# Optimization experiments

Measured on AMD Instinct MI355X. Metric: run time of the kernel, lower is better.

The kernel has to match this reference:

```python
import jax, jax.numpy as jnp
import numpy as np
import math

IMAGE_C = 1
IMAGE_W = 28
PIXELS_PER_ROW = IMAGE_W * IMAGE_C
NUM_HEADS = 8
TOP_K = 96
WINDOW_SIZE = 128
NEG_INF = -jnp.inf


def _causal_2d_mask(T):
    idx = jnp.arange(T)
    q_i = (idx // PIXELS_PER_ROW)[:, None]
    q_j = (idx % PIXELS_PER_ROW // IMAGE_C)[:, None]
    q_c = (idx % IMAGE_C)[:, None]
    k_i = (idx // PIXELS_PER_ROW)[None, :]
    k_j = (idx % PIXELS_PER_ROW // IMAGE_C)[None, :]
    k_c = (idx % IMAGE_C)[None, :]
    allowed = (k_i < q_i) | ((k_i == q_i) & (k_j < q_j)) | ((k_i == q_i) & (k_j == q_j) & (k_c <= q_c))
    return jnp.where(allowed, 0.0, NEG_INF)[None, None]  # [1,1,T,T]


def _window_mask(T, window_size):
    idx = jnp.arange(T)
    blocked = idx[None, :] < idx[:, None] - window_size + 1
    return jnp.where(blocked, NEG_INF, 0.0)[None, None]  # [1,1,T,T]


def setup_inputs() -> dict:
    key = jax.random.key(0)
    ks = jax.random.split(key, 10)
    B, T, E = 4, 2048, 512
    H = NUM_HEADS
    s = 0.02
    return {
        "x": jax.random.normal(ks[0], (B, T, E), jnp.float32),
        "Wq": jax.random.normal(ks[1], (E, E), jnp.float32) * s,
        "bq": jnp.zeros((E,), jnp.float32),
        "Wk": jax.random.normal(ks[2], (E, E), jnp.float32) * s,
        "bk": jnp.zeros((E,), jnp.float32),
        "Wv": jax.random.normal(ks[3], (E, E), jnp.float32) * s,
        "bv": jnp.zeros((E,), jnp.float32),
        "Wo": jax.random.normal(ks[4], (E, E), jnp.float32) * s,
        "bo": jnp.zeros((E,), jnp.float32),
        "log_sigma": jnp.full((H, 1, 1), math.log(2.5), jnp.float32),
    }


def reference(x, Wq, bq, Wk, bk, Wv, bv, Wo, bo, log_sigma):
    B, T, E = x.shape
    H = NUM_HEADS
    D = E // H

    def split_heads(y):  # [B,T,E] -> [B,H,T,D]
        return y.reshape(B, T, H, D).transpose(0, 2, 1, 3)

    q = split_heads(x @ Wq.T + bq)
    k = split_heads(x @ Wk.T + bk)
    v = split_heads(x @ Wv.T + bv)

    # Gaussian-kernel (squared-distance) scores: ||q-k||^2 / (-2 sigma^2)
    q_sq = jnp.sum(q * q, axis=-1, keepdims=True)            # [B,H,T,1]
    k_sq = jnp.sum(k * k, axis=-1, keepdims=True).transpose(0, 1, 3, 2)  # [B,H,1,T]
    product = jnp.einsum("bhqd,bhkd->bhqk", q, k)
    dist_sq = q_sq + k_sq - 2.0 * product
    sigma_sq = jnp.exp(2.0 * log_sigma)                       # [H,1,1]
    scores = dist_sq / (-2.0 * sigma_sq)

    scores = scores + _causal_2d_mask(T)
    if WINDOW_SIZE < T:
        scores = scores + _window_mask(T, WINDOW_SIZE)

    if TOP_K < T:
        K_val = min(TOP_K, T)
        # keep only the top-K scores per row (threshold at the K-th value);
        # equivalent to torch's gather/scatter for distinct finite scores
        top_vals = jax.lax.top_k(scores, K_val)[0]            # [B,H,T,K]
        kth = top_vals[..., -1:]
        scores = jnp.where(scores >= kth, scores, NEG_INF)

    probs = jax.nn.softmax(scores, axis=-1)                   # dropout = identity (eval)
    out = jnp.einsum("bhqk,bhkd->bhqd", probs, v)
    out = out.transpose(0, 2, 1, 3).reshape(B, T, E)
    return out @ Wo.T + bo
```

## Files before the change

kernel.cpp:

```cpp
#include <hip/hip_runtime.h>
#include <math.h>

#define T_SEQ   2048
#define EDIM    512
#define NHEADS  8
#define DHEAD   64
#define BATCH   4
#define WIN     128
#define TOPK    96

typedef _Float16 f16;
typedef f16 f16x2 __attribute__((ext_vector_type(2)));
typedef f16 f16x4 __attribute__((ext_vector_type(4)));
typedef f16 f16x8 __attribute__((ext_vector_type(8)));
typedef float f32x4 __attribute__((ext_vector_type(4)));

#define GLD_LDS(gp, lp) \
    __builtin_amdgcn_global_load_lds((const __attribute__((address_space(1))) void*)(gp), \
                                     (__attribute__((address_space(3))) void*)(lp), 16, 0, 0)

__global__ __launch_bounds__(256) void convert_all(
    const float* __restrict__ x,  const float* __restrict__ wq,
    const float* __restrict__ wk, const float* __restrict__ wv,
    const float* __restrict__ wo,
    f16* __restrict__ xh, f16* __restrict__ wqkvh, f16* __restrict__ woh)
{
    long i = ((long)blockIdx.x * 256 + threadIdx.x) * 4;
    const float* src; f16* dst; long off;
    if      (i < 4194304L) { src = x;  dst = xh;             off = i;            }
    else if (i < 4456448L) { src = wq; dst = wqkvh;          off = i - 4194304L; }
    else if (i < 4718592L) { src = wk; dst = wqkvh + 262144; off = i - 4456448L; }
    else if (i < 4980736L) { src = wv; dst = wqkvh + 524288; off = i - 4718592L; }
    else                   { src = wo; dst = woh;            off = i - 4980736L; }
    float4 v = *(const float4*)(src + off);
    f16x4 h; h.x = (f16)v.x; h.y = (f16)v.y; h.z = (f16)v.z; h.w = (f16)v.w;
    *(f16x4*)(dst + off) = h;
}

__global__ __launch_bounds__(256) void ksq_kernel(const f16* __restrict__ kh,
                                                  float* __restrict__ ksqg)
{
    const int i   = blockIdx.x * 256 + threadIdx.x;
    const int row = i >> 2, part = i & 3;
    const f16* p = kh + (size_t)row * 64 + part * 16;
    const f16x8 a = ((const f16x8*)p)[0];
    const f16x8 b = ((const f16x8*)p)[1];
    float s = 0.f;
#pragma unroll
    for (int j = 0; j < 8; j++) {
        const float fa = (float)a[j], fb = (float)b[j];
        s += fa * fa + fb * fb;
    }
    s += __shfl_xor(s, 1);
    s += __shfl_xor(s, 2);
    if (part == 0) ksqg[row] = s;
}

template <int MODE>
__global__ __launch_bounds__(256) void gemm_mfma(
    const f16* __restrict__ A, const f16* __restrict__ W,
    const float* __restrict__ b0, const float* __restrict__ b1,
    const float* __restrict__ b2, float* __restrict__ C0,
    f16* __restrict__ cq, f16* __restrict__ ck, f16* __restrict__ cv)
{
    __shared__ f16 Ash[16 * 512];
    __shared__ f16 Bsh[16 * 512];

    const int tid  = threadIdx.x;
    const int w    = tid >> 6;
    const int lane = tid & 63;
    const int m0   = blockIdx.x * 128;
    const int n0   = blockIdx.y * 128;
    const int K    = 512;
    const int lr   = lane & 15;
    const int lk8  = (lane >> 4) * 8;

    f32x4 acc[4][4];
#pragma unroll
    for (int i = 0; i < 4; i++)
#pragma unroll
        for (int j = 0; j < 4; j++) acc[i][j] = (f32x4){0.f, 0.f, 0.f, 0.f};

    const int wmi = (w & 1) * 4;
    const int wni = (w >> 1) * 4;

    for (int k0 = 0; k0 < K; k0 += 64) {
#pragma unroll
        for (int cc = 0; cc < 4; cc++) {
            const int c  = w * 4 + cc;
            const int ms = c & 7, kp = c >> 3;
            const int kcol = k0 + kp * 32 + lk8;
            GLD_LDS(A + (size_t)(m0 + ms * 16 + lr) * K + kcol, Ash + c * 512);
            GLD_LDS(W + (size_t)(n0 + ms * 16 + lr) * K + kcol, Bsh + c * 512);
        }
        __syncthreads();

#pragma unroll
        for (int kp = 0; kp < 2; kp++) {
            f16x8 af[4], bf[4];
#pragma unroll
            for (int i = 0; i < 4; i++)
                af[i] = *(const f16x8*)(Ash + (kp * 8 + wmi + i) * 512 + lane * 8);
#pragma unroll
            for (int j = 0; j < 4; j++)
                bf[j] = *(const f16x8*)(Bsh + (kp * 8 + wni + j) * 512 + lane * 8);
#pragma unroll
            for (int i = 0; i < 4; i++)
#pragma unroll
                for (int j = 0; j < 4; j++)
                    acc[i][j] = __builtin_amdgcn_mfma_f32_16x16x32_f16(af[i], bf[j], acc[i][j], 0, 0, 0);
        }
        __syncthreads();
    }

    const int quad = lane >> 4;
    if (MODE == 0) {
#pragma unroll
        for (int i = 0; i < 4; i++) {
#pragma unroll
            for (int j = 0; j < 4; j++) {
                const int n  = n0 + (w >> 1) * 64 + j * 16 + lr;
                const float bv = b0[n];
#pragma unroll
                for (int r = 0; r < 4; r++) {
                    const int m = m0 + (w & 1) * 64 + i * 16 + quad * 4 + r;
                    C0[(size_t)m * 512 + n] = acc[i][j][r] + bv;
                }
            }
        }
    } else {
        const int mat = n0 >> 9;
        const float* bias = (mat == 0) ? b0 : ((mat == 1) ? b1 : b2);
#pragma unroll
        for (int i = 0; i < 4; i++) {
#pragma unroll
            for (int j = 0; j < 4; j++) {
                const int n    = n0 + (w >> 1) * 64 + j * 16 + lr;
                const int ncol = n & 511;
                const int h    = ncol >> 6, d = ncol & 63;
                const float bv = bias[ncol];
                if (mat < 2) {
                    f16* dst = (mat == 0) ? cq : ck;
#pragma unroll
                    for (int r = 0; r < 4; r++) {
                        const int m = m0 + (w & 1) * 64 + i * 16 + quad * 4 + r;
                        const int b = m >> 11, t = m & (T_SEQ - 1);
                        dst[((size_t)((b * NHEADS + h) * T_SEQ) + t) * 64 + d] =
                            (f16)(acc[i][j][r] + bv);
                    }
                } else {
                    const int mb = m0 + (w & 1) * 64 + i * 16 + quad * 4;
                    const int b = mb >> 11, t = mb & (T_SEQ - 1);
                    f16x4 pk;
#pragma unroll
                    for (int r = 0; r < 4; r++) pk[r] = (f16)(acc[i][j][r] + bv);
                    *(f16x4*)(cv + ((size_t)((b * NHEADS + h) * 64 + d)) * T_SEQ + t) = pk;
                }
            }
        }
    }
}

__global__ __launch_bounds__(256) void attn_v3(
    const f16* __restrict__ qh, const f16* __restrict__ kh,
    const f16* __restrict__ vtg, const float* __restrict__ ksqg,
    const float* __restrict__ logsig, f16* __restrict__ abh)
{
    __shared__ __align__(16) char smem[75520];
    f16*   Qs   = (f16*)smem;
    f16*   Ks   = (f16*)(smem + 10240);
    f16*   P    = (f16*)smem;
    float* Sc   = (float*)(smem + 40960);
    f16*   Vt   = (f16*)(smem + 40960);
    float* ksqs = (float*)(smem + 74752);

    const int tid = threadIdx.x, w = tid >> 6, lane = tid & 63;
    const int lr = lane & 15, quad = lane >> 4;
    const int q0 = blockIdx.x * 64, bh = blockIdx.y;
    const int h = bh & 7, b = bh >> 3;
    const size_t tb = (size_t)bh * T_SEQ;
    const int ks0 = q0 - 128;

#pragma unroll
    for (int s = 0; s < 2; s++) {
        const int i = tid + 256 * s;
        const int row = i >> 3, ch = i & 7;
        f16x8 v = *(const f16x8*)(qh + (tb + q0 + row) * 64 + ch * 8);
        *(f16x8*)(Qs + row * 80 + ch * 8) = v;
    }
#pragma unroll
    for (int s = 0; s < 6; s++) {
        const int i = tid + 256 * s;
        const int row = i >> 3, ch = i & 7;
        const int kg = ks0 + row;
        f16x8 v = {};
        if (kg >= 0) v = *(const f16x8*)(kh + (tb + kg) * 64 + ch * 8);
        *(f16x8*)(Ks + row * 80 + ch * 8) = v;
    }
    if (tid < 192) {
        const int kg = ks0 + tid;
        ksqs[tid] = (kg >= 0) ? ksqg[tb + kg] : 0.f;
    }
    __syncthreads();

    f32x4 accQ[4][3];
#pragma unroll
    for (int i = 0; i < 4; i++)
#pragma unroll
        for (int jt = 0; jt < 3; jt++) accQ[i][jt] = (f32x4){0.f, 0.f, 0.f, 0.f};

    const int nb = w * 48;
#pragma unroll
    for (int kp = 0; kp < 2; kp++) {
        f16x8 bf[3];
#pragma unroll
        for (int jt = 0; jt < 3; jt++)
            bf[jt] = *(const f16x8*)(Ks + (nb + jt * 16 + lr) * 80 + kp * 32 + quad * 8);
#pragma unroll
        for (int i = 0; i < 4; i++) {
            const f16x8 af = *(const f16x8*)(Qs + (i * 16 + lr) * 80 + kp * 32 + quad * 8);
#pragma unroll
            for (int jt = 0; jt < 3; jt++)
                accQ[i][jt] = __builtin_amdgcn_mfma_f32_16x16x32_f16(af, bf[jt], accQ[i][jt], 0, 0, 0);
        }
    }
    const float inv_s2 = __expf(-2.0f * logsig[h]);
#pragma unroll
    for (int i = 0; i < 4; i++) {
#pragma unroll
        for (int jt = 0; jt < 3; jt++) {
            const int c  = nb + jt * 16 + lr;
            const float kq = ksqs[c];
            const int kg = ks0 + c;
#pragma unroll
            for (int r = 0; r < 4; r++) {
                const int dq = i * 16 + quad * 4 + r;
                const unsigned wc = (unsigned)(c - dq - 1);
                if (wc < 128u) {
                    const float sv = (kg >= 0) ? (accQ[i][jt][r] - 0.5f * kq) * inv_s2
                                               : -INFINITY;
                    Sc[dq * 132 + wc] = sv;
                }
            }
        }
    }
    __syncthreads();

    const int wq = w * 16;
#pragma unroll 1
    for (int qp = 0; qp < 8; qp++) {
        const int dqA = wq + qp * 2, dqB = dqA + 1;
        const float s0A = Sc[dqA * 132 + lane], s1A = Sc[dqA * 132 + 64 + lane];
        const float s0B = Sc[dqB * 132 + lane], s1B = Sc[dqB * 132 + 64 + lane];
        const unsigned b0A = __float_as_uint(s0A), b1A = __float_as_uint(s1A);
        const unsigned b0B = __float_as_uint(s0B), b1B = __float_as_uint(s1B);
        const unsigned u0A = b0A ^ (unsigned)(((int)b0A >> 31) | 0x80000000);
        const unsigned u1A = b1A ^ (unsigned)(((int)b1A >> 31) | 0x80000000);
        const unsigned u0B = b0B ^ (unsigned)(((int)b0B >> 31) | 0x80000000);
        const unsigned u1B = b1B ^ (unsigned)(((int)b1B >> 31) | 0x80000000);
        const float mA = __uint_as_float(__builtin_amdgcn_readlane(__float_as_uint(s1A), 63));
        const float mB = __uint_as_float(__builtin_amdgcn_readlane(__float_as_uint(s1B), 63));

        unsigned tA = 0u, tB = 0u;
#pragma unroll
        for (int bit = 31; bit >= 0; bit--) {
            const unsigned cA = tA | (1u << bit);
            const unsigned cB = tB | (1u << bit);
            const int nA = __popcll(__ballot(u0A >= cA)) + __popcll(__ballot(u1A >= cA));
            const int nB = __popcll(__ballot(u0B >= cB)) + __popcll(__ballot(u1B >= cB));
            if (nA >= TOPK) tA = cA;
            if (nB >= TOPK) tB = cB;
        }

        const float p0A = (u0A >= tA) ? __expf(s0A - mA) : 0.f;
        const float p1A = (u1A >= tA) ? __expf(s1A - mA) : 0.f;
        const float p0B = (u0B >= tB) ? __expf(s0B - mB) : 0.f;
        const float p1B = (u1B >= tB) ? __expf(s1B - mB) : 0.f;

        P[dqA * 200 + dqA + 1 + lane]  = (f16)p0A;
        P[dqA * 200 + dqA + 65 + lane] = (f16)p1A;
        P[dqA * 200 + ((lane <= dqA) ? lane : lane + 128)] = (f16)0.f;
        P[dqB * 200 + dqB + 1 + lane]  = (f16)p0B;
        P[dqB * 200 + dqB + 65 + lane] = (f16)p1B;
        P[dqB * 200 + ((lane <= dqB) ? lane : lane + 128)] = (f16)0.f;
    }
    __syncthreads();

#pragma unroll
    for (int s = 0; s < 6; s++) {
        const int i = tid + 256 * s;
        const int d = i / 24, ch = i % 24;
        const int t0 = ks0 + ch * 8;
        f16x8 vv = {};
        if (t0 >= 0) vv = *(const f16x8*)(vtg + ((size_t)bh * 64 + d) * T_SEQ + t0);
        *(f16x8*)(Vt + d * 200 + ch * 8) = vv;
    }
    __syncthreads();

    f32x4 accO[4];
#pragma unroll
    for (int nt = 0; nt < 4; nt++) accO[nt] = (f32x4){0.f, 0.f, 0.f, 0.f};
    f32x4 accS = (f32x4){0.f, 0.f, 0.f, 0.f};
    f16x8 onesf;
#pragma unroll
    for (int j = 0; j < 8; j++) onesf[j] = (f16)1.0f;

#pragma unroll
    for (int ks = 0; ks < 6; ks++) {
        const f16x8 pf = *(const f16x8*)(P + (wq + lr) * 200 + ks * 32 + quad * 8);
#pragma unroll
        for (int nt = 0; nt < 4; nt++) {
            const f16x8 vf = *(const f16x8*)(Vt + (nt * 16 + lr) * 200 + ks * 32 + quad * 8);
            accO[nt] = __builtin_amdgcn_mfma_f32_16x16x32_f16(pf, vf, accO[nt], 0, 0, 0);
        }
        accS = __builtin_amdgcn_mfma_f32_16x16x32_f16(pf, onesf, accS, 0, 0, 0);
    }
    float inv[4];
#pragma unroll
    for (int r = 0; r < 4; r++) inv[r] = 1.0f / accS[r];

#pragma unroll
    for (int nt = 0; nt < 4; nt++) {
        const int d = nt * 16 + lr;
#pragma unroll
        for (int r = 0; r < 4; r++) {
            const int q = q0 + wq + quad * 4 + r;
            abh[((size_t)(b * T_SEQ + q)) * 512 + h * 64 + d] = (f16)(accO[nt][r] * inv[r]);
        }
    }
}

extern "C" void kernel_launch(void* const* d_in, const int* in_sizes, int n_in,
                              void* d_out, int out_size, void* d_ws, size_t ws_size,
                              hipStream_t stream)
{
    const float* x      = (const float*)d_in[0];
    const float* Wq     = (const float*)d_in[1];
    const float* bq     = (const float*)d_in[2];
    const float* Wk     = (const float*)d_in[3];
    const float* bk     = (const float*)d_in[4];
    const float* Wv     = (const float*)d_in[5];
    const float* bv     = (const float*)d_in[6];
    const float* Wo     = (const float*)d_in[7];
    const float* bo     = (const float*)d_in[8];
    const float* logsig = (const float*)d_in[9];

    f16*   xh    = (f16*)d_ws;
    f16*   wqkvh = xh + 4194304;
    f16*   woh   = wqkvh + 786432;
    f16*   qh    = woh + 262144;
    f16*   kh    = qh + 4194304;
    f16*   vtg   = kh + 4194304;
    float* ksqg  = (float*)(vtg + 4194304);
    f16*   abh   = xh;

    convert_all<<<5120, 256, 0, stream>>>(x, Wq, Wk, Wv, Wo, xh, wqkvh, woh);

    gemm_mfma<1><<<dim3(64, 12), 256, 0, stream>>>(
        xh, wqkvh, bq, bk, bv, nullptr, qh, kh, vtg);

    ksq_kernel<<<1024, 256, 0, stream>>>(kh, ksqg);

    attn_v3<<<dim3(T_SEQ / 64, BATCH * NHEADS), 256, 0, stream>>>(
        qh, kh, vtg, ksqg, logsig, abh);

    gemm_mfma<0><<<dim3(64, 4), 256, 0, stream>>>(
        abh, woh, bo, nullptr, nullptr, (float*)d_out, nullptr, nullptr, nullptr);
}
```

Measured before the change: 192.0 us.

## Fuse k-norm into attention, double attention threads, narrow output GEMM tiles

Removes the separate ksq kernel by computing squared key norms while staging K tiles inside the attention kernel. The attention block grows from 256 to 512 threads. Each wave now handles one query tile and half of the key or value columns, and runs the top-k bisection on four rows at once for more independent ballots. LDS row strides are padded (80→88, 200→216) to cut bank conflicts. The output projection gets its own kernel with 128x64 tiles, doubling the grid for better CU occupancy, at the cost of more A-tile reloads.

```diff
diff --git a/kernel.cpp b/kernel.cpp
--- a/kernel.cpp
+++ b/kernel.cpp
@@ -37,30 +37,10 @@
     *(f16x4*)(dst + off) = h;
 }
 
-__global__ __launch_bounds__(256) void ksq_kernel(const f16* __restrict__ kh,
-                                                  float* __restrict__ ksqg)
-{
-    const int i   = blockIdx.x * 256 + threadIdx.x;
-    const int row = i >> 2, part = i & 3;
-    const f16* p = kh + (size_t)row * 64 + part * 16;
-    const f16x8 a = ((const f16x8*)p)[0];
-    const f16x8 b = ((const f16x8*)p)[1];
-    float s = 0.f;
-#pragma unroll
-    for (int j = 0; j < 8; j++) {
-        const float fa = (float)a[j], fb = (float)b[j];
-        s += fa * fa + fb * fb;
-    }
-    s += __shfl_xor(s, 1);
-    s += __shfl_xor(s, 2);
-    if (part == 0) ksqg[row] = s;
-}
-
-template <int MODE>
-__global__ __launch_bounds__(256) void gemm_mfma(
+__global__ __launch_bounds__(256) void gemm_qkv(
     const f16* __restrict__ A, const f16* __restrict__ W,
     const float* __restrict__ b0, const float* __restrict__ b1,
-    const float* __restrict__ b2, float* __restrict__ C0,
+    const float* __restrict__ b2,
     f16* __restrict__ cq, f16* __restrict__ ck, f16* __restrict__ cv)
 {
     __shared__ f16 Ash[16 * 512];
@@ -114,65 +94,119 @@
     }
 
     const int quad = lane >> 4;
-    if (MODE == 0) {
-#pragma unroll
-        for (int i = 0; i < 4; i++) {
-#pragma unroll
-            for (int j = 0; j < 4; j++) {
-                const int n  = n0 + (w >> 1) * 64 + j * 16 + lr;
-                const float bv = b0[n];
+    const int mat = n0 >> 9;
+    const float* bias = (mat == 0) ? b0 : ((mat == 1) ? b1 : b2);
+#pragma unroll
+    for (int i = 0; i < 4; i++) {
+#pragma unroll
+        for (int j = 0; j < 4; j++) {
+            const int n    = n0 + (w >> 1) * 64 + j * 16 + lr;
+            const int ncol = n & 511;
+            const int h    = ncol >> 6, d = ncol & 63;
+            const float bv = bias[ncol];
+            if (mat < 2) {
+                f16* dst = (mat == 0) ? cq : ck;
 #pragma unroll
                 for (int r = 0; r < 4; r++) {
                     const int m = m0 + (w & 1) * 64 + i * 16 + quad * 4 + r;
-                    C0[(size_t)m * 512 + n] = acc[i][j][r] + bv;
+                    const int b = m >> 11, t = m & (T_SEQ - 1);
+                    dst[((size_t)((b * NHEADS + h) * T_SEQ) + t) * 64 + d] =
+                        (f16)(acc[i][j][r] + bv);
                 }
+            } else {
+                const int mb = m0 + (w & 1) * 64 + i * 16 + quad * 4;
+                const int b = mb >> 11, t = mb & (T_SEQ - 1);
+                f16x4 pk;
+#pragma unroll
+                for (int r = 0; r < 4; r++) pk[r] = (f16)(acc[i][j][r] + bv);
+                *(f16x4*)(cv + ((size_t)((b * NHEADS + h) * 64 + d)) * T_SEQ + t) = pk;
             }
         }
-    } else {
-        const int mat = n0 >> 9;
-        const float* bias = (mat == 0) ? b0 : ((mat == 1) ? b1 : b2);
-#pragma unroll
-        for (int i = 0; i < 4; i++) {
-#pragma unroll
-            for (int j = 0; j < 4; j++) {
-                const int n    = n0 + (w >> 1) * 64 + j * 16 + lr;
-                const int ncol = n & 511;
-                const int h    = ncol >> 6, d = ncol & 63;
-                const float bv = bias[ncol];
-                if (mat < 2) {
-                    f16* dst = (mat == 0) ? cq : ck;
-#pragma unroll
-                    for (int r = 0; r < 4; r++) {
-                        const int m = m0 + (w & 1) * 64 + i * 16 + quad * 4 + r;
-                        const int b = m >> 11, t = m & (T_SEQ - 1);
-                        dst[((size_t)((b * NHEADS + h) * T_SEQ) + t) * 64 + d] =
-                            (f16)(acc[i][j][r] + bv);
-                    }
-                } else {
-                    const int mb = m0 + (w & 1) * 64 + i * 16 + quad * 4;
-                    const int b = mb >> 11, t = mb & (T_SEQ - 1);
-                    f16x4 pk;
-#pragma unroll
-                    for (int r = 0; r < 4; r++) pk[r] = (f16)(acc[i][j][r] + bv);
-                    *(f16x4*)(cv + ((size_t)((b * NHEADS + h) * 64 + d)) * T_SEQ + t) = pk;
-                }
+    }
+}
+
+__global__ __launch_bounds__(256) void gemm_o(
+    const f16* __restrict__ A, const f16* __restrict__ W,
+    const float* __restrict__ bias, float* __restrict__ C)
+{
+    __shared__ f16 Ash[16 * 512];
+    __shared__ f16 Bsh[8 * 512];
+
+    const int tid  = threadIdx.x;
+    const int w    = tid >> 6;
+    const int lane = tid & 63;
+    const int m0   = blockIdx.x * 128;
+    const int n0   = blockIdx.y * 64;
+    const int lr   = lane & 15;
+    const int lk8  = (lane >> 4) * 8;
+
+    f32x4 acc[4][2];
+#pragma unroll
+    for (int i = 0; i < 4; i++)
+#pragma unroll
+        for (int j = 0; j < 2; j++) acc[i][j] = (f32x4){0.f, 0.f, 0.f, 0.f};
+
+    for (int k0 = 0; k0 < 512; k0 += 64) {
+#pragma unroll
+        for (int cc = 0; cc < 4; cc++) {
+            const int c  = w * 4 + cc;
+            const int ms = c & 7, kp = c >> 3;
+            GLD_LDS(A + (size_t)(m0 + ms * 16 + lr) * 512 + k0 + kp * 32 + lk8, Ash + c * 512);
+        }
+#pragma unroll
+        for (int cc = 0; cc < 2; cc++) {
+            const int c  = w * 2 + cc;
+            const int ns = c & 3, kp = c >> 2;
+            GLD_LDS(W + (size_t)(n0 + ns * 16 + lr) * 512 + k0 + kp * 32 + lk8, Bsh + c * 512);
+        }
+        __syncthreads();
+
+#pragma unroll
+        for (int kp = 0; kp < 2; kp++) {
+            f16x8 af[4], bf[2];
+#pragma unroll
+            for (int i = 0; i < 4; i++)
+                af[i] = *(const f16x8*)(Ash + (kp * 8 + (w & 1) * 4 + i) * 512 + lane * 8);
+#pragma unroll
+            for (int j = 0; j < 2; j++)
+                bf[j] = *(const f16x8*)(Bsh + (kp * 4 + (w >> 1) * 2 + j) * 512 + lane * 8);
+#pragma unroll
+            for (int i = 0; i < 4; i++)
+#pragma unroll
+                for (int j = 0; j < 2; j++)
+                    acc[i][j] = __builtin_amdgcn_mfma_f32_16x16x32_f16(af[i], bf[j], acc[i][j], 0, 0, 0);
+        }
+        __syncthreads();
+    }
+
+    const int quad = lane >> 4;
+#pragma unroll
+    for (int i = 0; i < 4; i++) {
+#pragma unroll
+        for (int j = 0; j < 2; j++) {
+            const int n  = n0 + (w >> 1) * 32 + j * 16 + lr;
+            const float bv = bias[n];
+#pragma unroll
+            for (int r = 0; r < 4; r++) {
+                const int m = m0 + (w & 1) * 64 + i * 16 + quad * 4 + r;
+                C[(size_t)m * 512 + n] = acc[i][j][r] + bv;
             }
         }
     }
 }
 
-__global__ __launch_bounds__(256) void attn_v3(
+__global__ __launch_bounds__(512, 4) void attn_v4(
     const f16* __restrict__ qh, const f16* __restrict__ kh,
-    const f16* __restrict__ vtg, const float* __restrict__ ksqg,
-    const float* __restrict__ logsig, f16* __restrict__ abh)
-{
-    __shared__ __align__(16) char smem[75520];
+    const f16* __restrict__ vtg, const float* __restrict__ logsig,
+    f16* __restrict__ abh)
+{
+    __shared__ __align__(16) char smem[79616];
     f16*   Qs   = (f16*)smem;
-    f16*   Ks   = (f16*)(smem + 10240);
+    f16*   Ks   = (f16*)(smem + 11264);
     f16*   P    = (f16*)smem;
-    float* Sc   = (float*)(smem + 40960);
-    f16*   Vt   = (f16*)(smem + 40960);
-    float* ksqs = (float*)(smem + 74752);
+    float* Sc   = (float*)(smem + 45056);
+    f16*   Vt   = (f16*)(smem + 45056);
+    float* ksqs = (float*)(smem + 78848);
 
     const int tid = threadIdx.x, w = tid >> 6, lane = tid & 63;
     const int lr = lane & 15, quad = lane >> 4;
@@ -181,125 +215,117 @@
     const size_t tb = (size_t)bh * T_SEQ;
     const int ks0 = q0 - 128;
 
-#pragma unroll
-    for (int s = 0; s < 2; s++) {
-        const int i = tid + 256 * s;
-        const int row = i >> 3, ch = i & 7;
+    {
+        const int row = tid >> 3, ch = tid & 7;
         f16x8 v = *(const f16x8*)(qh + (tb + q0 + row) * 64 + ch * 8);
-        *(f16x8*)(Qs + row * 80 + ch * 8) = v;
-    }
-#pragma unroll
-    for (int s = 0; s < 6; s++) {
-        const int i = tid + 256 * s;
+        *(f16x8*)(Qs + row * 88 + ch * 8) = v;
+    }
+#pragma unroll
+    for (int s = 0; s < 3; s++) {
+        const int i = tid + 512 * s;
         const int row = i >> 3, ch = i & 7;
         const int kg = ks0 + row;
         f16x8 v = {};
         if (kg >= 0) v = *(const f16x8*)(kh + (tb + kg) * 64 + ch * 8);
-        *(f16x8*)(Ks + row * 80 + ch * 8) = v;
-    }
-    if (tid < 192) {
-        const int kg = ks0 + tid;
-        ksqs[tid] = (kg >= 0) ? ksqg[tb + kg] : 0.f;
+        *(f16x8*)(Ks + row * 88 + ch * 8) = v;
+        float ps = 0.f;
+#pragma unroll
+        for (int j = 0; j < 8; j++) { const float fv = (float)v[j]; ps += fv * fv; }
+        ps += __shfl_xor(ps, 1);
+        ps += __shfl_xor(ps, 2);
+        ps += __shfl_xor(ps, 4);
+        if (ch == 0) ksqs[row] = ps;
     }
     __syncthreads();
 
-    f32x4 accQ[4][3];
-#pragma unroll
-    for (int i = 0; i < 4; i++)
-#pragma unroll
-        for (int jt = 0; jt < 3; jt++) accQ[i][jt] = (f32x4){0.f, 0.f, 0.f, 0.f};
-
-    const int nb = w * 48;
+    const int mt  = w & 3;
+    const int kh2 = w >> 2;
+    f32x4 accQ[6];
+#pragma unroll
+    for (int jt = 0; jt < 6; jt++) accQ[jt] = (f32x4){0.f, 0.f, 0.f, 0.f};
+
 #pragma unroll
     for (int kp = 0; kp < 2; kp++) {
-        f16x8 bf[3];
-#pragma unroll
-        for (int jt = 0; jt < 3; jt++)
-            bf[jt] = *(const f16x8*)(Ks + (nb + jt * 16 + lr) * 80 + kp * 32 + quad * 8);
-#pragma unroll
-        for (int i = 0; i < 4; i++) {
-            const f16x8 af = *(const f16x8*)(Qs + (i * 16 + lr) * 80 + kp * 32 + quad * 8);
-#pragma unroll
-            for (int jt = 0; jt < 3; jt++)
-                accQ[i][jt] = __builtin_amdgcn_mfma_f32_16x16x32_f16(af, bf[jt], accQ[i][jt], 0, 0, 0);
+        const f16x8 af = *(const f16x8*)(Qs + (mt * 16 + lr) * 88 + kp * 32 + quad * 8);
+#pragma unroll
+        for (int jt = 0; jt < 6; jt++) {
+            const f16x8 bf = *(const f16x8*)(Ks + (kh2 * 96 + jt * 16 + lr) * 88 + kp * 32 + quad * 8);
+            accQ[jt] = __builtin_amdgcn_mfma_f32_16x16x32_f16(af, bf, accQ[jt], 0, 0, 0);
         }
     }
     const float inv_s2 = __expf(-2.0f * logsig[h]);
 #pragma unroll
-    for (int i = 0; i < 4; i++) {
-#pragma unroll
-        for (int jt = 0; jt < 3; jt++) {
-            const int c  = nb + jt * 16 + lr;
-            const float kq = ksqs[c];
-            const int kg = ks0 + c;
-#pragma unroll
-            for (int r = 0; r < 4; r++) {
-                const int dq = i * 16 + quad * 4 + r;
-                const unsigned wc = (unsigned)(c - dq - 1);
-                if (wc < 128u) {
-                    const float sv = (kg >= 0) ? (accQ[i][jt][r] - 0.5f * kq) * inv_s2
-                                               : -INFINITY;
-                    Sc[dq * 132 + wc] = sv;
-                }
+    for (int jt = 0; jt < 6; jt++) {
+        const int c  = kh2 * 96 + jt * 16 + lr;
+        const float kq = ksqs[c];
+        const int kg = ks0 + c;
+#pragma unroll
+        for (int r = 0; r < 4; r++) {
+            const int dq = mt * 16 + quad * 4 + r;
+            const unsigned wc = (unsigned)(c - dq - 1);
+            if (wc < 128u) {
+                Sc[dq * 132 + wc] = (kg >= 0) ? (accQ[jt][r] - 0.5f * kq) * inv_s2
+                                              : -INFINITY;
             }
         }
     }
     __syncthreads();
 
-    const int wq = w * 16;
+    const int wq8 = w * 8;
 #pragma unroll 1
-    for (int qp = 0; qp < 8; qp++) {
-        const int dqA = wq + qp * 2, dqB = dqA + 1;
-        const float s0A = Sc[dqA * 132 + lane], s1A = Sc[dqA * 132 + 64 + lane];
-        const float s0B = Sc[dqB * 132 + lane], s1B = Sc[dqB * 132 + 64 + lane];
-        const unsigned b0A = __float_as_uint(s0A), b1A = __float_as_uint(s1A);
-        const unsigned b0B = __float_as_uint(s0B), b1B = __float_as_uint(s1B);
-        const unsigned u0A = b0A ^ (unsigned)(((int)b0A >> 31) | 0x80000000);
-        const unsigned u1A = b1A ^ (unsigned)(((int)b1A >> 31) | 0x80000000);
-        const unsigned u0B = b0B ^ (unsigned)(((int)b0B >> 31) | 0x80000000);
-        const unsigned u1B = b1B ^ (unsigned)(((int)b1B >> 31) | 0x80000000);
-        const float mA = __uint_as_float(__builtin_amdgcn_readlane(__float_as_uint(s1A), 63));
-        const float mB = __uint_as_float(__builtin_amdgcn_readlane(__float_as_uint(s1B), 63));
-
-        unsigned tA = 0u, tB = 0u;
+    for (int g = 0; g < 2; g++) {
+        const int dq0 = wq8 + g * 4;
+        float s0[4], s1[4], m[4];
+        unsigned u0[4], u1[4], t[4];
+#pragma unroll
+        for (int qq = 0; qq < 4; qq++) {
+            const int dq = dq0 + qq;
+            s0[qq] = Sc[dq * 132 + lane];
+            s1[qq] = Sc[dq * 132 + 64 + lane];
+            const unsigned b0 = __float_as_uint(s0[qq]);
+            const unsigned b1 = __float_as_uint(s1[qq]);
+            u0[qq] = b0 ^ (unsigned)(((int)b0 >> 31) | 0x80000000);
+            u1[qq] = b1 ^ (unsigned)(((int)b1 >> 31) | 0x80000000);
+            m[qq] = __uint_as_float(__builtin_amdgcn_readlane(__float_as_uint(s1[qq]), 63));
+            t[qq] = 0u;
+        }
 #pragma unroll
         for (int bit = 31; bit >= 0; bit--) {
-            const unsigned cA = tA | (1u << bit);
-            const unsigned cB = tB | (1u << bit);
-            const int nA = __popcll(__ballot(u0A >= cA)) + __popcll(__ballot(u1A >= cA));
-            const int nB = __popcll(__ballot(u0B >= cB)) + __popcll(__ballot(u1B >= cB));
-            if (nA >= TOPK) tA = cA;
-            if (nB >= TOPK) tB = cB;
-        }
-
-        const float p0A = (u0A >= tA) ? __expf(s0A - mA) : 0.f;
-        const float p1A = (u1A >= tA) ? __expf(s1A - mA) : 0.f;
-        const float p0B = (u0B >= tB) ? __expf(s0B - mB) : 0.f;
-        const float p1B = (u1B >= tB) ? __expf(s1B - mB) : 0.f;
-
-        P[dqA * 200 + dqA + 1 + lane]  = (f16)p0A;
-        P[dqA * 200 + dqA + 65 + lane] = (f16)p1A;
-        P[dqA * 200 + ((lane <= dqA) ? lane : lane + 128)] = (f16)0.f;
-        P[dqB * 200 + dqB + 1 + lane]  = (f16)p0B;
-        P[dqB * 200 + dqB + 65 + lane] = (f16)p1B;
-        P[dqB * 200 + ((lane <= dqB) ? lane : lane + 128)] = (f16)0.f;
+#pragma unroll
+            for (int qq = 0; qq < 4; qq++) {
+                const unsigned c = t[qq] | (1u << bit);
+                const int n = __popcll(__ballot(u0[qq] >= c)) +
+                              __popcll(__ballot(u1[qq] >= c));
+                if (n >= TOPK) t[qq] = c;
+            }
+        }
+#pragma unroll
+        for (int qq = 0; qq < 4; qq++) {
+            const int dq = dq0 + qq;
+            const float p0 = (u0[qq] >= t[qq]) ? __expf(s0[qq] - m[qq]) : 0.f;
+            const float p1 = (u1[qq] >= t[qq]) ? __expf(s1[qq] - m[qq]) : 0.f;
+            P[dq * 216 + dq + 1 + lane]  = (f16)p0;
+            P[dq * 216 + dq + 65 + lane] = (f16)p1;
+            P[dq * 216 + ((lane <= dq) ? lane : lane + 128)] = (f16)0.f;
+        }
     }
     __syncthreads();
 
 #pragma unroll
-    for (int s = 0; s < 6; s++) {
-        const int i = tid + 256 * s;
+    for (int s = 0; s < 3; s++) {
+        const int i = tid + 512 * s;
         const int d = i / 24, ch = i % 24;
         const int t0 = ks0 + ch * 8;
         f16x8 vv = {};
         if (t0 >= 0) vv = *(const f16x8*)(vtg + ((size_t)bh * 64 + d) * T_SEQ + t0);
-        *(f16x8*)(Vt + d * 200 + ch * 8) = vv;
+        *(f16x8*)(Vt + d * 216 + ch * 8) = vv;
     }
     __syncthreads();
 
-    f32x4 accO[4];
-#pragma unroll
-    for (int nt = 0; nt < 4; nt++) accO[nt] = (f32x4){0.f, 0.f, 0.f, 0.f};
+    const int nh = w >> 2;
+    f32x4 accO[2];
+#pragma unroll
+    for (int nt = 0; nt < 2; nt++) accO[nt] = (f32x4){0.f, 0.f, 0.f, 0.f};
     f32x4 accS = (f32x4){0.f, 0.f, 0.f, 0.f};
     f16x8 onesf;
 #pragma unroll
@@ -307,10 +333,10 @@
 
 #pragma unroll
     for (int ks = 0; ks < 6; ks++) {
-        const f16x8 pf = *(const f16x8*)(P + (wq + lr) * 200 + ks * 32 + quad * 8);
-#pragma unroll
-        for (int nt = 0; nt < 4; nt++) {
-            const f16x8 vf = *(const f16x8*)(Vt + (nt * 16 + lr) * 200 + ks * 32 + quad * 8);
+        const f16x8 pf = *(const f16x8*)(P + (mt * 16 + lr) * 216 + ks * 32 + quad * 8);
+#pragma unroll
+        for (int nt = 0; nt < 2; nt++) {
+            const f16x8 vf = *(const f16x8*)(Vt + (nh * 32 + nt * 16 + lr) * 216 + ks * 32 + quad * 8);
             accO[nt] = __builtin_amdgcn_mfma_f32_16x16x32_f16(pf, vf, accO[nt], 0, 0, 0);
         }
         accS = __builtin_amdgcn_mfma_f32_16x16x32_f16(pf, onesf, accS, 0, 0, 0);
@@ -320,11 +346,11 @@
     for (int r = 0; r < 4; r++) inv[r] = 1.0f / accS[r];
 
 #pragma unroll
-    for (int nt = 0; nt < 4; nt++) {
-        const int d = nt * 16 + lr;
+    for (int nt = 0; nt < 2; nt++) {
+        const int d = nh * 32 + nt * 16 + lr;
 #pragma unroll
         for (int r = 0; r < 4; r++) {
-            const int q = q0 + wq + quad * 4 + r;
+            const int q = q0 + mt * 16 + quad * 4 + r;
             abh[((size_t)(b * T_SEQ + q)) * 512 + h * 64 + d] = (f16)(accO[nt][r] * inv[r]);
         }
     }
@@ -345,25 +371,20 @@
     const float* bo     = (const float*)d_in[8];
     const float* logsig = (const float*)d_in[9];
 
-    f16*   xh    = (f16*)d_ws;
-    f16*   wqkvh = xh + 4194304;
-    f16*   woh   = wqkvh + 786432;
-    f16*   qh    = woh + 262144;
-    f16*   kh    = qh + 4194304;
-    f16*   vtg   = kh + 4194304;
-    float* ksqg  = (float*)(vtg + 4194304);
-    f16*   abh   = xh;
+    f16* xh    = (f16*)d_ws;
+    f16* wqkvh = xh + 4194304;
+    f16* woh   = wqkvh + 786432;
+    f16* qh    = woh + 262144;
+    f16* kh    = qh + 4194304;
+    f16* vtg   = kh + 4194304;
+    f16* abh   = xh;
 
     convert_all<<<5120, 256, 0, stream>>>(x, Wq, Wk, Wv, Wo, xh, wqkvh, woh);
 
-    gemm_mfma<1><<<dim3(64, 12), 256, 0, stream>>>(
-        xh, wqkvh, bq, bk, bv, nullptr, qh, kh, vtg);
-
-    ksq_kernel<<<1024, 256, 0, stream>>>(kh, ksqg);
-
-    attn_v3<<<dim3(T_SEQ / 64, BATCH * NHEADS), 256, 0, stream>>>(
-        qh, kh, vtg, ksqg, logsig, abh);
-
-    gemm_mfma<0><<<dim3(64, 4), 256, 0, stream>>>(
-        abh, woh, bo, nullptr, nullptr, (float*)d_out, nullptr, nullptr, nullptr);
-}
+    gemm_qkv<<<dim3(64, 12), 256, 0, stream>>>(xh, wqkvh, bq, bk, bv, qh, kh, vtg);
+
+    attn_v4<<<dim3(T_SEQ / 64, BATCH * NHEADS), 512, 0, stream>>>(
+        qh, kh, vtg, logsig, abh);
+
+    gemm_o<<<dim3(64, 8), 256, 0, stream>>>(abh, woh, bo, (float*)d_out);
+}
```

Measured after the change: 177.4 us. -7.6%, faster.
